# Kernel tuning notes

Measured on AMD Instinct MI355X. Metric: run time of the kernel, lower is better.

The kernel has to match this reference:

```python
import jax, jax.numpy as jnp
import numpy as np

B, N, G = 32, 262144, 256


def setup_inputs() -> dict:
    key = jax.random.key(0)
    k1, k2, k3 = jax.random.split(key, 3)
    pr = jax.random.normal(k1, (B, N), dtype=jnp.float32)
    inp_means = jax.random.normal(k2, (B, G), dtype=jnp.float32)
    vr = jax.random.randint(k3, (B, N, 1), 0, G, dtype=jnp.int32)
    W = jnp.ones((2,), dtype=jnp.float32)  # hist_weight, ones initializer
    return {"pr": pr, "inp_means": inp_means, "vr": vr, "W": W}


def reference(pr, inp_means, vr, W):
    sg = jax.lax.stop_gradient
    G = inp_means.shape[1]
    v = jnp.squeeze(vr, -1)  # [B, N] int cluster ids (stop_gradient in orig; int anyway)
    p_sg = sg(pr)

    # Per-batch segmented min/max/sum/any over clusters (replaces python loop over g).
    def seg(p, psg, vi):
        mn = jnp.full((G,), jnp.inf, p.dtype).at[vi].min(psg)    # min(where(gidx, pr, inf))
        mx = jnp.full((G,), -jnp.inf, p.dtype).at[vi].max(psg)   # max(where(gidx, pr, -inf))
        sm = jnp.zeros((G,), p.dtype).at[vi].add(p)              # sum(where(gidx, pr, 0))
        any_ = jnp.zeros((G,), bool).at[vi].set(True)            # reduce_any(gidx)
        return mn, mx, sm, any_

    vmins, vmaxs, vsum, vany = jax.vmap(seg)(pr, p_sg, v)  # each [B, G]
    # Original divides sum by cast(any)->1.0 (or 0/0=nan -> 0), i.e. the group SUM.
    vmeans = jnp.where(vany, vsum, jnp.zeros((), pr.dtype))
    vmeans = (inp_means * W[0] + vmeans * W[1]) / (W[0] + W[1])

    no_scale = vmins == vmaxs  # [B, G]
    vmins_g = jnp.take_along_axis(jnp.where(no_scale, 0.0, vmins), v, axis=1)  # [B, N]
    vmaxs_g = jnp.take_along_axis(jnp.where(no_scale, 1.0, vmaxs), v, axis=1)  # [B, N]

    sort_ids = jnp.argsort(vmeans, axis=1)
    orig_ids = jnp.argsort(sort_ids, axis=1)  # inverse permutation
    vs = jnp.take_along_axis(vmeans, sort_ids, axis=1)  # [B, G]
    cd = jnp.concatenate([vs[:, :1], vs, vs[:, -1:] * 2], axis=1)  # [B, G+2]
    # conv1d with kernel ones(2)/c, VALID: out[i] = (cd[i] + cd[i+1]) / c
    f0 = (cd[:, :-2] + cd[:, 1:-1]) / 1.999  # conv(...)[:, :-1]
    f1 = (cd[:, 1:-1] + cd[:, 2:]) / 2.001   # conv(...)[:, 1:]
    f0 = jnp.take_along_axis(
        jnp.where(no_scale, 0.0, jnp.take_along_axis(f0, orig_ids, axis=1)), v, axis=1)
    f1 = jnp.take_along_axis(
        jnp.where(no_scale, 1.0, jnp.take_along_axis(f1, orig_ids, axis=1)), v, axis=1)

    tmp = (sg(pr) - sg(vmins_g)) / sg(vmaxs_g - vmins_g) * (f1 - f0) + f0  # [B, N]
    bad = jnp.isnan(tmp) | (tmp == 0.0)
    s = pr / jnp.where(bad, 1.0, tmp)  # safe denominator (grad-safe)
    scale = jnp.where(bad | jnp.isnan(s) | jnp.isinf(s), 0.0, s)
    return pr * scale
```

## Files before the change

### kernel.cpp

```cpp
#include <hip/hip_runtime.h>
#include <math.h>

#define NB 32
#define NN 262144
#define NG 256
#define NC 64
#define CH (NN/NC)
#define SC (CH/4)
#define CD 64
#define ELD (NN/CD)

__global__ __launch_bounds__(256) void k_count(const int* __restrict__ vr,
                                               unsigned* __restrict__ cnt,
                                               unsigned* __restrict__ gid32){
  __shared__ unsigned scnt[NG];
  const int t = threadIdx.x;
  scnt[t] = 0u;
  __syncthreads();

  const int b = blockIdx.x / NC;
  const int c = blockIdx.x % NC;
  const size_t base = (size_t)b*NN + (size_t)c*CH;
  const int4* v4 = (const int4*)(vr + base);

#pragma unroll
  for (int i = 0; i < CH/1024; i++){
    int4 v = v4[i*256 + t];
    atomicAdd(&scnt[v.x], 1u);
    atomicAdd(&scnt[v.y], 1u);
    atomicAdd(&scnt[v.z], 1u);
    atomicAdd(&scnt[v.w], 1u);
    gid32[(base >> 2) + i*256 + t] =
      (unsigned)v.x | ((unsigned)v.y << 8) | ((unsigned)v.z << 16) | ((unsigned)v.w << 24);
  }
  __syncthreads();
  cnt[(size_t)(b*NC + c)*NG + t] = scnt[t];
}

__global__ __launch_bounds__(256) void k_offsets(unsigned* __restrict__ cnt,
                                                 unsigned* __restrict__ grpbase,
                                                 unsigned* __restrict__ grplen){
  const int b = blockIdx.x;
  const int g = threadIdx.x;

  unsigned v[NC];
#pragma unroll
  for (int c = 0; c < NC; c++) v[c] = cnt[(size_t)(b*NC + c)*NG + g];
  unsigned tot = 0;
#pragma unroll
  for (int c = 0; c < NC; c++) tot += v[c];

  __shared__ unsigned ss[NG];
  ss[g] = tot; __syncthreads();
  for (int d = 1; d < NG; d <<= 1){
    unsigned x = (g >= d) ? ss[g - d] : 0u;
    __syncthreads();
    ss[g] += x;
    __syncthreads();
  }
  unsigned base = ss[g] - tot;

  unsigned run = base;
#pragma unroll
  for (int c = 0; c < NC; c++){
    cnt[(size_t)(b*NC + c)*NG + g] = run;
    run += v[c];
  }
  grpbase[b*NG + g] = base;
  grplen [b*NG + g] = tot;
}

__global__ __launch_bounds__(256) void k_scatter(const float* __restrict__ pr,
                                                 const unsigned* __restrict__ gid32,
                                                 const unsigned* __restrict__ off,
                                                 float* __restrict__ sorted){
  __shared__ float vbuf[CH];
  __shared__ unsigned graw32[CH/4];
  __shared__ unsigned char gbuf[CH];
  __shared__ unsigned wcnt[4][NG];
  __shared__ unsigned bias[NG];
  __shared__ unsigned ss[NG];
  const int t    = threadIdx.x;
  const int lane = t & 63;
  const int w    = t >> 6;
  const int b = blockIdx.x / NC;
  const int c = blockIdx.x % NC;
  const size_t base = (size_t)b*NN + (size_t)c*CH;

#pragma unroll
  for (int k = 0; k < 4; k++) wcnt[k][t] = 0u;
  __syncthreads();

  {
    const uint4* g4 = (const uint4*)(gid32 + (base >> 2));
    uint4 pk = g4[w*64 + lane];
    ((uint4*)graw32)[w*64 + lane] = pk;
#define HIST4(P) { atomicAdd(&wcnt[w][(P) & 255u], 1u); \
                   atomicAdd(&wcnt[w][((P) >> 8) & 255u], 1u); \
                   atomicAdd(&wcnt[w][((P) >> 16) & 255u], 1u); \
                   atomicAdd(&wcnt[w][(P) >> 24], 1u); }
    HIST4(pk.x) HIST4(pk.y) HIST4(pk.z) HIST4(pk.w)
#undef HIST4
  }
  __syncthreads();

  {
    unsigned c0 = wcnt[0][t], c1 = wcnt[1][t], c2 = wcnt[2][t], c3 = wcnt[3][t];
    unsigned tot = c0 + c1 + c2 + c3;
    ss[t] = tot; __syncthreads();
    for (int d = 1; d < NG; d <<= 1){
      unsigned v = (t >= d) ? ss[t - d] : 0u;
      __syncthreads();
      ss[t] += v;
      __syncthreads();
    }
    unsigned lb = ss[t] - tot;
    wcnt[0][t] = lb;
    wcnt[1][t] = lb + c0;
    wcnt[2][t] = lb + c0 + c1;
    wcnt[3][t] = lb + c0 + c1 + c2;
    bias[t] = off[(size_t)(b*NC + c)*NG + t] - lb;
  }
  __syncthreads();

  {
    const unsigned long long below = (lane == 0) ? 0ull : ((1ull << lane) - 1ull);
    const float* psrc = pr + base + (size_t)w*SC;
    const int shft = (lane & 3) * 8;
    for (int s = 0; s < SC/64; s++){
      float p = psrc[s*64 + lane];
      unsigned packed = graw32[w*(SC/4) + s*16 + (lane >> 2)];
      int g = (int)((packed >> shft) & 255u);
      unsigned long long mask = ~0ull;
#pragma unroll
      for (int bit = 0; bit < 8; bit++){
        int bv = (g >> bit) & 1;
        unsigned long long bal = __ballot(bv);
        mask &= bv ? bal : ~bal;
      }
      int rank = __popcll(mask & below);
      unsigned old = wcnt[w][g];
      if (rank == 0) wcnt[w][g] = old + (unsigned)__popcll(mask);
      vbuf[old + (unsigned)rank] = p;
      gbuf[old + (unsigned)rank] = (unsigned char)g;
    }
  }
  __syncthreads();

  {
    float* dst = sorted + (size_t)b*NN;
    const unsigned* gbuf32 = (const unsigned*)gbuf;
#pragma unroll
    for (int k = 0; k < CH/256; k++){
      int p = k*256 + t;
      unsigned packed = gbuf32[p >> 2];
      unsigned g = (packed >> ((p & 3) * 8)) & 255u;
      dst[bias[g] + (unsigned)p] = vbuf[p];
    }
  }
}

__global__ __launch_bounds__(32) void k_sum(const float* __restrict__ sorted,
                                            const unsigned* __restrict__ grpbase,
                                            const unsigned* __restrict__ grplen,
                                            float* __restrict__ gsum,
                                            float* __restrict__ gmn,
                                            float* __restrict__ gmx){
  const int lane = threadIdx.x;
  const int b = blockIdx.x >> 3;
  const int g = ((blockIdx.x & 7) << 5) + lane;

  const unsigned base = grpbase[b*NG + g];
  const unsigned len  = grplen [b*NG + g];
  const float* sp = sorted + (size_t)b*NN + base;

  float s = 0.0f, mn = INFINITY, mx = -INFINITY;

  unsigned head = (4u - ((unsigned)(((size_t)sp) >> 2) & 3u)) & 3u;
  if (head > len) head = len;
  for (unsigned i = 0; i < head; i++){
    float v = sp[i];
    s = __fadd_rn(s, v); mn = fminf(mn, v); mx = fmaxf(mx, v);
  }
  const float4* f4 = (const float4*)(sp + head);
  const unsigned rem   = len - head;
  const unsigned nfull = rem >> 4;

  float4 b0[4], b1[4], b2[4], b3[4], b4[4], b5[4], b6[4], b7[4];
#define LOADV(D, K) { D[0]=f4[(K)*4+0]; D[1]=f4[(K)*4+1]; D[2]=f4[(K)*4+2]; D[3]=f4[(K)*4+3]; }
#define CONS1(V)    { s=__fadd_rn(s,(V)); mn=fminf(mn,(V)); mx=fmaxf(mx,(V)); }
#define CONSV(D)    { _Pragma("unroll") for (int j = 0; j < 4; j++){ float4 q = D[j]; \
                      CONS1(q.x) CONS1(q.y) CONS1(q.z) CONS1(q.w) } }

  if (nfull > 0) LOADV(b0, 0)
  if (nfull > 1) LOADV(b1, 1)
  if (nfull > 2) LOADV(b2, 2)
  if (nfull > 3) LOADV(b3, 3)
  if (nfull > 4) LOADV(b4, 4)
  if (nfull > 5) LOADV(b5, 5)
  if (nfull > 6) LOADV(b6, 6)
  if (nfull > 7) LOADV(b7, 7)
  unsigned k = 0;
  for (; k + 8 <= nfull; k += 8){
    CONSV(b0) if (k +  8 < nfull) LOADV(b0, k +  8)
    CONSV(b1) if (k +  9 < nfull) LOADV(b1, k +  9)
    CONSV(b2) if (k + 10 < nfull) LOADV(b2, k + 10)
    CONSV(b3) if (k + 11 < nfull) LOADV(b3, k + 11)
    CONSV(b4) if (k + 12 < nfull) LOADV(b4, k + 12)
    CONSV(b5) if (k + 13 < nfull) LOADV(b5, k + 13)
    CONSV(b6) if (k + 14 < nfull) LOADV(b6, k + 14)
    CONSV(b7) if (k + 15 < nfull) LOADV(b7, k + 15)
  }
  {
    unsigned r = nfull - k;
    if (r > 0) CONSV(b0)
    if (r > 1) CONSV(b1)
    if (r > 2) CONSV(b2)
    if (r > 3) CONSV(b3)
    if (r > 4) CONSV(b4)
    if (r > 5) CONSV(b5)
    if (r > 6) CONSV(b6)
  }
  for (unsigned i = head + (nfull << 4); i < len; i++){
    float v = sp[i];
    s = __fadd_rn(s, v); mn = fminf(mn, v); mx = fmaxf(mx, v);
  }
#undef LOADV
#undef CONS1
#undef CONSV

  gsum[b*NG + g] = s;
  gmn [b*NG + g] = mn;
  gmx [b*NG + g] = mx;
}

__global__ __launch_bounds__(256) void k_pipeline(const float* __restrict__ gsum,
                                                  const float* __restrict__ gmn,
                                                  const float* __restrict__ gmx,
                                                  const float* __restrict__ inp_means,
                                                  const float* __restrict__ Wv,
                                                  float* __restrict__ params){
  const int b = blockIdx.x;
  const int g = threadIdx.x;
  __shared__ float vm[NG];
  __shared__ float vs[NG];

  const float s   = gsum[b*NG + g];
  const float mnf = gmn [b*NG + g];
  const float mxf = gmx [b*NG + g];
  const float W0 = Wv[0], W1 = Wv[1];
  float mean = __fdiv_rn(__fadd_rn(__fmul_rn(inp_means[b*NG + g], W0),
                                   __fmul_rn(s, W1)),
                         __fadd_rn(W0, W1));
  vm[g] = mean;
  __syncthreads();

  int r = 0;
  for (int j = 0; j < NG; j++){
    float x = vm[j];
    r += (x < mean) || (x == mean && j < g);
  }
  vs[r] = mean;
  __syncthreads();

  float c0 = (r == 0)    ? vs[0]                     : vs[r-1];
  float c1 = vs[r];
  float c2 = (r == NG-1) ? __fmul_rn(vs[NG-1], 2.0f) : vs[r+1];
  float f0 = __fdiv_rn(__fadd_rn(c0, c1), 1.999f);
  float f1 = __fdiv_rn(__fadd_rn(c1, c2), 2.001f);

  bool ns = (mnf == mxf);
  params[(b*4 + 0)*NG + g] = ns ? 0.0f : mnf;
  params[(b*4 + 1)*NG + g] = ns ? 1.0f : __fsub_rn(mxf, mnf);
  params[(b*4 + 2)*NG + g] = ns ? 1.0f : __fsub_rn(f1, f0);
  params[(b*4 + 3)*NG + g] = ns ? 0.0f : f0;
}

static __device__ __forceinline__ float apply_one(float p, unsigned g,
                                                  const float* __restrict__ sp0,
                                                  const float* __restrict__ sp1,
                                                  const float* __restrict__ sp2,
                                                  const float* __restrict__ sp3){
  float t1  = __fsub_rn(p, sp0[g]);
  float t3  = __fdiv_rn(t1, sp1[g]);
  float t5  = __fmul_rn(t3, sp2[g]);
  float tmp = __fadd_rn(t5, sp3[g]);
  bool bad = __builtin_isnan(tmp) || (tmp == 0.0f);
  float s = __fdiv_rn(p, bad ? 1.0f : tmp);
  bool bad2 = bad || __builtin_isnan(s) || __builtin_isinf(s);
  float sc = bad2 ? 0.0f : s;
  return __fmul_rn(p, sc);
}

__global__ __launch_bounds__(256) void k_apply(const float* __restrict__ pr,
                                               const unsigned* __restrict__ gid32,
                                               const float* __restrict__ params,
                                               float* __restrict__ out){
  __shared__ float sp0[NG], sp1[NG], sp2[NG], sp3[NG];
  const int t = threadIdx.x;
  const int b = blockIdx.x / CD;
  const int c = blockIdx.x % CD;

  sp0[t] = params[(b*4 + 0)*NG + t];
  sp1[t] = params[(b*4 + 1)*NG + t];
  sp2[t] = params[(b*4 + 2)*NG + t];
  sp3[t] = params[(b*4 + 3)*NG + t];
  __syncthreads();

  const size_t base = (size_t)b*NN + (size_t)c*ELD;
  const float4* p4 = (const float4*)(pr + base);
  float4* o4 = (float4*)(out + base);

#pragma unroll
  for (int i = 0; i < ELD/1024; i++){
    float4 p = p4[i*256 + t];
    unsigned pk = gid32[(base >> 2) + i*256 + t];
    float4 r;
    r.x = apply_one(p.x,  pk        & 255u, sp0, sp1, sp2, sp3);
    r.y = apply_one(p.y, (pk >>  8) & 255u, sp0, sp1, sp2, sp3);
    r.z = apply_one(p.z, (pk >> 16) & 255u, sp0, sp1, sp2, sp3);
    r.w = apply_one(p.w,  pk >> 24,         sp0, sp1, sp2, sp3);
    o4[i*256 + t] = r;
  }
}

extern "C" void kernel_launch(void* const* d_in, const int* in_sizes, int n_in,
                              void* d_out, int out_size, void* d_ws, size_t ws_size,
                              hipStream_t stream){
  const float* pr        = (const float*)d_in[0];
  const float* inp_means = (const float*)d_in[1];
  const int*   vr        = (const int*)d_in[2];
  const float* W         = (const float*)d_in[3];
  float* out = (float*)d_out;

  char* ws = (char*)d_ws;
  size_t o = 0;
  unsigned* cnt     = (unsigned*)(ws + o); o += (size_t)NB*NC*NG*4;
  unsigned* gid32   = (unsigned*)(ws + o); o += (size_t)NB*NN;
  unsigned* grpbase = (unsigned*)(ws + o); o += (size_t)NB*NG*4;
  unsigned* grplen  = (unsigned*)(ws + o); o += (size_t)NB*NG*4;
  float*    gsum    = (float*)   (ws + o); o += (size_t)NB*NG*4;
  float*    gmn     = (float*)   (ws + o); o += (size_t)NB*NG*4;
  float*    gmx     = (float*)   (ws + o); o += (size_t)NB*NG*4;
  float*    params  = (float*)   (ws + o); o += (size_t)NB*NG*16;
  float* sorted = out;

  k_count   <<<NB*NC, 256, 0, stream>>>(vr, cnt, gid32);
  k_offsets <<<NB,     NG, 0, stream>>>(cnt, grpbase, grplen);
  k_scatter <<<NB*NC, 256, 0, stream>>>(pr, gid32, cnt, sorted);
  k_sum     <<<NB*8,   32, 0, stream>>>(sorted, grpbase, grplen, gsum, gmn, gmx);
  k_pipeline<<<NB,     NG, 0, stream>>>(gsum, gmn, gmx, inp_means, W, params);
  k_apply   <<<NB*CD, 256, 0, stream>>>(pr, gid32, params, out);
}
```

Baseline: 176.2 us.

## Compute per-wave histograms once in count kernel and reuse them in scatter

The count kernel now builds four per-wave histograms and stores them packed as four 16-bit counts in a 64-bit word. The scatter kernel reads these instead of recomputing its own histogram with shared atomics, and replaces the block-wide shared-memory scan with a wave shuffle scan plus a cross-wave fixup. Scatter also preloads 16 values and packed ids into registers before the ballot loop. The cost is a larger count buffer (8 bytes per entry) plus an extra read in offsets and scatter, and higher register pressure in scatter.

```diff
diff --git a/kernel.cpp b/kernel.cpp
--- a/kernel.cpp
+++ b/kernel.cpp
@@ -11,11 +11,13 @@
 #define ELD (NN/CD)
 
 __global__ __launch_bounds__(256) void k_count(const int* __restrict__ vr,
-                                               unsigned* __restrict__ cnt,
+                                               unsigned long long* __restrict__ wcnt16,
                                                unsigned* __restrict__ gid32){
-  __shared__ unsigned scnt[NG];
-  const int t = threadIdx.x;
-  scnt[t] = 0u;
+  __shared__ unsigned sc[4][NG];
+  const int t    = threadIdx.x;
+  const int lane = t & 63;
+  const int w    = t >> 6;
+  sc[0][t] = 0u; sc[1][t] = 0u; sc[2][t] = 0u; sc[3][t] = 0u;
   __syncthreads();
 
   const int b = blockIdx.x / NC;
@@ -24,20 +26,28 @@
   const int4* v4 = (const int4*)(vr + base);
 
 #pragma unroll
-  for (int i = 0; i < CH/1024; i++){
-    int4 v = v4[i*256 + t];
-    atomicAdd(&scnt[v.x], 1u);
-    atomicAdd(&scnt[v.y], 1u);
-    atomicAdd(&scnt[v.z], 1u);
-    atomicAdd(&scnt[v.w], 1u);
-    gid32[(base >> 2) + i*256 + t] =
+  for (int i = 0; i < 4; i++){
+    int idx = w*256 + i*64 + lane;
+    int4 v = v4[idx];
+    atomicAdd(&sc[w][v.x], 1u);
+    atomicAdd(&sc[w][v.y], 1u);
+    atomicAdd(&sc[w][v.z], 1u);
+    atomicAdd(&sc[w][v.w], 1u);
+    gid32[(base >> 2) + idx] =
       (unsigned)v.x | ((unsigned)v.y << 8) | ((unsigned)v.z << 16) | ((unsigned)v.w << 24);
   }
   __syncthreads();
-  cnt[(size_t)(b*NC + c)*NG + t] = scnt[t];
-}
-
-__global__ __launch_bounds__(256) void k_offsets(unsigned* __restrict__ cnt,
+
+  unsigned c0 = sc[0][t], c1 = sc[1][t], c2 = sc[2][t], c3 = sc[3][t];
+  const size_t cb = (size_t)b*NC + c;
+  wcnt16[cb*NG + t] = (unsigned long long)c0
+                    | ((unsigned long long)c1 << 16)
+                    | ((unsigned long long)c2 << 32)
+                    | ((unsigned long long)c3 << 48);
+}
+
+__global__ __launch_bounds__(256) void k_offsets(const unsigned long long* __restrict__ wcnt16,
+                                                 unsigned* __restrict__ off,
                                                  unsigned* __restrict__ grpbase,
                                                  unsigned* __restrict__ grplen){
   const int b = blockIdx.x;
@@ -45,7 +55,11 @@
 
   unsigned v[NC];
 #pragma unroll
-  for (int c = 0; c < NC; c++) v[c] = cnt[(size_t)(b*NC + c)*NG + g];
+  for (int c = 0; c < NC; c++){
+    unsigned long long x = wcnt16[(size_t)(b*NC + c)*NG + g];
+    unsigned lo = (unsigned)x, hi = (unsigned)(x >> 32);
+    v[c] = (lo & 0xFFFFu) + (lo >> 16) + (hi & 0xFFFFu) + (hi >> 16);
+  }
   unsigned tot = 0;
 #pragma unroll
   for (int c = 0; c < NC; c++) tot += v[c];
@@ -63,7 +77,7 @@
   unsigned run = base;
 #pragma unroll
   for (int c = 0; c < NC; c++){
-    cnt[(size_t)(b*NC + c)*NG + g] = run;
+    off[(size_t)(b*NC + c)*NG + g] = run;
     run += v[c];
   }
   grpbase[b*NG + g] = base;
@@ -73,64 +87,63 @@
 __global__ __launch_bounds__(256) void k_scatter(const float* __restrict__ pr,
                                                  const unsigned* __restrict__ gid32,
                                                  const unsigned* __restrict__ off,
+                                                 const unsigned long long* __restrict__ wcnt16,
                                                  float* __restrict__ sorted){
   __shared__ float vbuf[CH];
-  __shared__ unsigned graw32[CH/4];
   __shared__ unsigned char gbuf[CH];
   __shared__ unsigned wcnt[4][NG];
   __shared__ unsigned bias[NG];
-  __shared__ unsigned ss[NG];
+  __shared__ unsigned wsum[4];
   const int t    = threadIdx.x;
   const int lane = t & 63;
   const int w    = t >> 6;
   const int b = blockIdx.x / NC;
   const int c = blockIdx.x % NC;
   const size_t base = (size_t)b*NN + (size_t)c*CH;
-
-#pragma unroll
-  for (int k = 0; k < 4; k++) wcnt[k][t] = 0u;
-  __syncthreads();
+  const size_t cb   = (size_t)b*NC + c;
 
   {
-    const uint4* g4 = (const uint4*)(gid32 + (base >> 2));
-    uint4 pk = g4[w*64 + lane];
-    ((uint4*)graw32)[w*64 + lane] = pk;
-#define HIST4(P) { atomicAdd(&wcnt[w][(P) & 255u], 1u); \
-                   atomicAdd(&wcnt[w][((P) >> 8) & 255u], 1u); \
-                   atomicAdd(&wcnt[w][((P) >> 16) & 255u], 1u); \
-                   atomicAdd(&wcnt[w][(P) >> 24], 1u); }
-    HIST4(pk.x) HIST4(pk.y) HIST4(pk.z) HIST4(pk.w)
-#undef HIST4
-  }
-  __syncthreads();
-
-  {
-    unsigned c0 = wcnt[0][t], c1 = wcnt[1][t], c2 = wcnt[2][t], c3 = wcnt[3][t];
-    unsigned tot = c0 + c1 + c2 + c3;
-    ss[t] = tot; __syncthreads();
-    for (int d = 1; d < NG; d <<= 1){
-      unsigned v = (t >= d) ? ss[t - d] : 0u;
-      __syncthreads();
-      ss[t] += v;
-      __syncthreads();
+    unsigned long long x = wcnt16[cb*NG + t];
+    unsigned offt = off[cb*NG + t];
+    unsigned lo = (unsigned)x, hi = (unsigned)(x >> 32);
+    unsigned w0 = lo & 0xFFFFu, w1 = lo >> 16, w2 = hi & 0xFFFFu, w3 = hi >> 16;
+    unsigned tot = w0 + w1 + w2 + w3;
+
+    unsigned v = tot;
+#pragma unroll
+    for (int d = 1; d < 64; d <<= 1){
+      unsigned y = __shfl_up(v, d, 64);
+      if (lane >= d) v += y;
     }
-    unsigned lb = ss[t] - tot;
+    if (lane == 63) wsum[w] = v;
+    __syncthreads();
+    unsigned pre = 0;
+#pragma unroll
+    for (int k = 0; k < 3; k++) if (k < w) pre += wsum[k];
+    unsigned lb = pre + v - tot;
     wcnt[0][t] = lb;
-    wcnt[1][t] = lb + c0;
-    wcnt[2][t] = lb + c0 + c1;
-    wcnt[3][t] = lb + c0 + c1 + c2;
-    bias[t] = off[(size_t)(b*NC + c)*NG + t] - lb;
+    wcnt[1][t] = lb + w0;
+    wcnt[2][t] = lb + w0 + w1;
+    wcnt[3][t] = lb + w0 + w1 + w2;
+    bias[t] = offt - lb;
   }
   __syncthreads();
 
   {
     const unsigned long long below = (lane == 0) ? 0ull : ((1ull << lane) - 1ull);
-    const float* psrc = pr + base + (size_t)w*SC;
+    const float*    psrc = pr    + base        + (size_t)w*SC;
+    const unsigned* gsrc = gid32 + (base >> 2) + (size_t)w*(SC/4);
     const int shft = (lane & 3) * 8;
-    for (int s = 0; s < SC/64; s++){
-      float p = psrc[s*64 + lane];
-      unsigned packed = graw32[w*(SC/4) + s*16 + (lane >> 2)];
-      int g = (int)((packed >> shft) & 255u);
+
+    float pv[16]; unsigned pk[16];
+#pragma unroll
+    for (int s = 0; s < 16; s++){
+      pv[s] = psrc[s*64 + lane];
+      pk[s] = gsrc[s*16 + (lane >> 2)];
+    }
+#pragma unroll
+    for (int s = 0; s < 16; s++){
+      int g = (int)((pk[s] >> shft) & 255u);
       unsigned long long mask = ~0ull;
 #pragma unroll
       for (int bit = 0; bit < 8; bit++){
@@ -141,7 +154,7 @@
       int rank = __popcll(mask & below);
       unsigned old = wcnt[w][g];
       if (rank == 0) wcnt[w][g] = old + (unsigned)__popcll(mask);
-      vbuf[old + (unsigned)rank] = p;
+      vbuf[old + (unsigned)rank] = pv[s];
       gbuf[old + (unsigned)rank] = (unsigned char)g;
     }
   }
@@ -335,7 +348,8 @@
 
   char* ws = (char*)d_ws;
   size_t o = 0;
-  unsigned* cnt     = (unsigned*)(ws + o); o += (size_t)NB*NC*NG*4;
+  unsigned long long* wcnt16 = (unsigned long long*)(ws + o); o += (size_t)NB*NC*NG*8;
+  unsigned* off     = (unsigned*)(ws + o); o += (size_t)NB*NC*NG*4;
   unsigned* gid32   = (unsigned*)(ws + o); o += (size_t)NB*NN;
   unsigned* grpbase = (unsigned*)(ws + o); o += (size_t)NB*NG*4;
   unsigned* grplen  = (unsigned*)(ws + o); o += (size_t)NB*NG*4;
@@ -345,9 +359,9 @@
   float*    params  = (float*)   (ws + o); o += (size_t)NB*NG*16;
   float* sorted = out;
 
-  k_count   <<<NB*NC, 256, 0, stream>>>(vr, cnt, gid32);
-  k_offsets <<<NB,     NG, 0, stream>>>(cnt, grpbase, grplen);
-  k_scatter <<<NB*NC, 256, 0, stream>>>(pr, gid32, cnt, sorted);
+  k_count   <<<NB*NC, 256, 0, stream>>>(vr, wcnt16, gid32);
+  k_offsets <<<NB,     NG, 0, stream>>>(wcnt16, off, grpbase, grplen);
+  k_scatter <<<NB*NC, 256, 0, stream>>>(pr, gid32, off, wcnt16, sorted);
   k_sum     <<<NB*8,   32, 0, stream>>>(sorted, grpbase, grplen, gsum, gmn, gmx);
   k_pipeline<<<NB,     NG, 0, stream>>>(gsum, gmn, gmx, inp_means, W, params);
   k_apply   <<<NB*CD, 256, 0, stream>>>(pr, gid32, params, out);
```

Measured after the change: 173.0 us. About the same (-1.8%).
